# Kernel optimization log

Measured on AMD Instinct MI355X. Metric: run time of the kernel, lower is better.

The kernel has to match this reference:

```python
import jax, jax.numpy as jnp
import numpy as np

NUM_CLASSES = 80
INF = 1e8
STRIDES = (8, 16, 32, 64, 128)
REG = ((0.0, 64.0), (64.0, 128.0), (128.0, 256.0), (256.0, 512.0), (512.0, INF))
GRAY_F = (0.9, 1.1)
FM = ((128, 128), (64, 64), (32, 32), (16, 16), (8, 8))  # 1024x1024 input


def _build_level_constants():
    pts, rr, gr, st = [], [], [], []
    for (h, w), s, (lo, up) in zip(FM, STRIDES, REG):
        xs = np.arange(w, dtype=np.float32) * s
        ys = np.arange(h, dtype=np.float32) * s
        ym, xm = np.meshgrid(ys, xs, indexing='ij')
        n = h * w
        pts.append(np.stack([xm.ravel(), ym.ravel()], axis=-1))
        rr.append(np.tile(np.array([lo, up], np.float32), (n, 1)))
        gr.append(np.tile(np.array([lo * GRAY_F[0], up * GRAY_F[1]], np.float32), (n, 1)))
        st.append(np.full((n,), s, np.float32))
    cat = lambda a: jnp.asarray(np.concatenate(a, axis=0))
    return cat(pts), cat(rr), cat(gr), cat(st)


def setup_inputs() -> dict:
    key = jax.random.key(0)
    k1, k2, k3, k4 = jax.random.split(key, 4)
    B, G = 8, 100
    x0 = jax.random.uniform(k1, (B, G, 1), minval=0.0, maxval=900.0)
    y0 = jax.random.uniform(k2, (B, G, 1), minval=0.0, maxval=900.0)
    wh = jax.random.uniform(k3, (B, G, 2), minval=8.0, maxval=512.0)
    gt_bboxes = jnp.concatenate([x0, y0, wh], axis=-1)  # xywh
    gt_labels = jax.random.randint(k4, (B, G), 0, NUM_CLASSES)
    points, reg_ranges, gray_ranges, strides = _build_level_constants()
    return dict(gt_bboxes=gt_bboxes, gt_labels=gt_labels, points=points,
                reg_ranges=reg_ranges, gray_ranges=gray_ranges, strides=strides)


def _single_image(gt_bboxes, gt_labels, points, reg_ranges, gray_ranges, strides):
    # gt_bboxes [G,4] (x,y,w,h); points [P,2]; returns [P, C+4]
    px = points[:, 0:1]                      # [P,1]
    py = points[:, 1:2]
    x0 = gt_bboxes[None, :, 0]               # [1,G]
    y0 = gt_bboxes[None, :, 1]
    w = gt_bboxes[None, :, 2]
    h = gt_bboxes[None, :, 3]
    cx = x0 + w / 2.0
    cy = y0 + h / 2.0
    half = strides[:, None] / 2.0            # [P,1]

    xs = jnp.abs(px - cx) / half
    xs = jnp.where(xs >= 1.0, xs, 1.0)       # == xs*(xs>=1) + (xs<1)
    ys = jnp.abs(py - cy) / half
    ys = jnp.where(ys >= 1.0, ys, 1.0)
    scores = jnp.sqrt(1.0 / xs) * jnp.sqrt(1.0 / ys)   # [P,G]

    dx1 = px - x0
    dy1 = py - y0
    dx2 = x0 + w - 1.0 - px
    dy2 = y0 + h - 1.0 - py
    delta = jnp.stack([dx1, dy1, dx2, dy2], axis=-1)   # [P,G,4]
    delta = delta / reg_ranges[:, 1][:, None, None]

    larger = jnp.maximum(w, h)               # [1,G]
    lo, up = reg_ranges[:, 0:1], reg_ranges[:, 1:2]      # [P,1]
    glo, gup = gray_ranges[:, 0:1], gray_ranges[:, 1:2]
    hit = jnp.min(delta, axis=-1) >= 0       # [P,G]
    green = (lo <= larger) & (larger <= up) & hit
    gray = (((glo <= larger) & (larger < lo)) | ((up < larger) & (larger <= gup))) & hit

    order = jnp.argsort(scores, axis=1)      # ascending, like torch.sort
    s_scores = jnp.take_along_axis(scores, order, axis=1)
    s_labels = jnp.take_along_axis(jnp.broadcast_to(gt_labels[None, :], scores.shape), order, axis=1)
    s_green = jnp.take_along_axis(green, order, axis=1)
    s_gray = jnp.take_along_axis(gray, order, axis=1)
    s_delta = jnp.take_along_axis(delta, order[..., None], axis=1)

    P = points.shape[0]
    rows = jnp.broadcast_to(jnp.arange(P)[:, None], s_labels.shape)
    cls = jnp.zeros((P, NUM_CLASSES), scores.dtype)
    cls = cls.at[rows, s_labels].max(jnp.where(s_green, s_scores, 0.0))
    gray_hit = jnp.zeros((P, NUM_CLASSES), scores.dtype)
    gray_hit = gray_hit.at[rows, s_labels].max(s_gray.astype(scores.dtype))
    cls = jnp.where(gray_hit > 0, -1.0, cls)  # gray writes happen after green

    filt = s_scores * (s_green & ~s_gray)
    sel = jnp.argmax(filt, axis=1)            # first max, like torch.max
    reg = jnp.take_along_axis(s_delta, sel[:, None, None], axis=1)[:, 0, :]  # [P,4]
    return jnp.concatenate([cls, reg], axis=-1)


def reference(gt_bboxes, gt_labels, points, reg_ranges, gray_ranges, strides):
    f = jax.vmap(lambda b, l: _single_image(b, l, points, reg_ranges, gray_ranges, strides))
    return f(gt_bboxes, gt_labels)
```

## Files before the change

kernel.cpp:

```cpp
#include <hip/hip_runtime.h>

#define ROWF 84

__global__ __launch_bounds__(64) void lfd_assign_kernel(
    const float* __restrict__ gt_bboxes,
    const int*   __restrict__ gt_labels,
    const float* __restrict__ points,
    const float* __restrict__ reg_ranges,
    const float* __restrict__ gray_ranges,
    const float* __restrict__ strides,
    float* __restrict__ out,
    int G, int P)
{
    extern __shared__ float lds[];
    float4*   boxA  = (float4*)lds;
    float2*   ctr   = (float2*)(boxA + G);
    unsigned* clist = (unsigned*)(ctr + ((G + 1) & ~1));

    const int tid = threadIdx.x;
    const int b   = blockIdx.y;
    const int p   = blockIdx.x * 64 + tid;

    const float px  = points[p * 2 + 0];
    const float py  = points[p * 2 + 1];
    const float lo  = reg_ranges[p * 2 + 0];
    const float up  = reg_ranges[p * 2 + 1];
    const float glo = gray_ranges[p * 2 + 0];
    const float gup = gray_ranges[p * 2 + 1];
    const float inv_half = 2.0f / strides[p];
    const float inv_up   = 1.0f / up;

    bool i0 = false, gray0 = false, i1 = false, gray1 = false;
    int  lab0 = 0, lab1 = 0;
    {
        int g = tid;
        if (g < G) {
            const float4 bb = *(const float4*)(gt_bboxes + (size_t)(b * G + g) * 4);
            boxA[g] = make_float4(bb.x, bb.y, bb.x + bb.z - 1.0f, bb.y + bb.w - 1.0f);
            ctr[g]  = make_float2(bb.x + 0.5f * bb.z, bb.y + 0.5f * bb.w);
            const float larger = fmaxf(bb.z, bb.w);
            lab0 = gt_labels[b * G + g];
            const bool green = (lo <= larger) && (larger <= up);
            gray0 = ((glo <= larger) && (larger < lo)) || ((up < larger) && (larger <= gup));
            i0 = green || gray0;
        }
        g = tid + 64;
        if (g < G) {
            const float4 bb = *(const float4*)(gt_bboxes + (size_t)(b * G + g) * 4);
            boxA[g] = make_float4(bb.x, bb.y, bb.x + bb.z - 1.0f, bb.y + bb.w - 1.0f);
            ctr[g]  = make_float2(bb.x + 0.5f * bb.z, bb.y + 0.5f * bb.w);
            const float larger = fmaxf(bb.z, bb.w);
            lab1 = gt_labels[b * G + g];
            const bool green = (lo <= larger) && (larger <= up);
            gray1 = ((glo <= larger) && (larger < lo)) || ((up < larger) && (larger <= gup));
            i1 = green || gray1;
        }
    }
    const unsigned long long m0 = __ballot(i0);
    const unsigned long long m1 = __ballot(i1);
    const int c0 = __popcll(m0);
    const unsigned long long below = (1ull << tid) - 1ull;
    if (i0) clist[__popcll(m0 & below)] =
        (unsigned)tid | ((unsigned)lab0 << 8) | (gray0 ? 0x80000000u : 0u);
    if (i1) clist[c0 + __popcll(m1 & below)] =
        (unsigned)(tid + 64) | ((unsigned)lab1 << 8) | (gray1 ? 0x80000000u : 0u);
    const int ncomp = c0 + __popcll(m1);

    float4* dst4 = (float4*)(out + (size_t)(b * P + blockIdx.x * 64) * ROWF);
    const float4 z4 = make_float4(0.f, 0.f, 0.f, 0.f);
#pragma unroll
    for (int k = 0; k < 21; ++k)
        dst4[k * 64 + tid] = z4;

    const float4* ctr2 = (const float4*)ctr;
    float min_score = 1e30f; int min_g = 0;
    int g = 0;
#pragma unroll 4
    for (; g + 1 < G; g += 2) {
        const float4 c = ctr2[g >> 1];
        const float s0 = rsqrtf(fmaxf(fabsf(px - c.x) * inv_half, 1.0f) *
                                fmaxf(fabsf(py - c.y) * inv_half, 1.0f));
        const float s1 = rsqrtf(fmaxf(fabsf(px - c.z) * inv_half, 1.0f) *
                                fmaxf(fabsf(py - c.w) * inv_half, 1.0f));
        if (s0 < min_score) { min_score = s0; min_g = g; }
        if (s1 < min_score) { min_score = s1; min_g = g + 1; }
    }
    if (g < G) {
        const float2 c = ctr[g];
        const float s0 = rsqrtf(fmaxf(fabsf(px - c.x) * inv_half, 1.0f) *
                                fmaxf(fabsf(py - c.y) * inv_half, 1.0f));
        if (s0 < min_score) { min_score = s0; min_g = g; }
    }

    asm volatile("s_waitcnt vmcnt(0)" ::: "memory");

    float* myout = out + (size_t)(b * P + p) * ROWF;
    float best_score = 0.0f; int best_g = 0;
    unsigned gm0 = 0u, gm1 = 0u, gm2 = 0u;
    for (int i = 0; i < ncomp; ++i) {
        const unsigned e = clist[i];
        const int gg = (int)(e & 0xFFu);
        const float4 A = boxA[gg];
        const float d1 = px - A.x, d2 = py - A.y, d3 = A.z - px, d4 = A.w - py;
        if (fminf(fminf(d1, d2), fminf(d3, d4)) >= 0.0f) {
            const int label = (int)((e >> 8) & 0x7Fu);
            if (e & 0x80000000u) {
                if (label < 32)      gm0 |= 1u << label;
                else if (label < 64) gm1 |= 1u << (label - 32);
                else                 gm2 |= 1u << (label - 64);
            } else {
                const float2 c = ctr[gg];
                const float s = rsqrtf(fmaxf(fabsf(px - c.x) * inv_half, 1.0f) *
                                       fmaxf(fabsf(py - c.y) * inv_half, 1.0f));
                atomicMax((int*)(myout + label), __float_as_int(s));
                if (s > best_score) { best_score = s; best_g = gg; }
            }
        }
    }

    asm volatile("s_waitcnt vmcnt(0)" ::: "memory");

    while (gm0) { const int c = __ffs(gm0) - 1; myout[c]      = -1.0f; gm0 &= gm0 - 1u; }
    while (gm1) { const int c = __ffs(gm1) - 1; myout[32 + c] = -1.0f; gm1 &= gm1 - 1u; }
    while (gm2) { const int c = __ffs(gm2) - 1; myout[64 + c] = -1.0f; gm2 &= gm2 - 1u; }

    const int sel = (best_score > 0.0f) ? best_g : min_g;
    const float4 A = boxA[sel];
    *(float4*)(myout + 80) = make_float4((px - A.x) * inv_up, (py - A.y) * inv_up,
                                         (A.z - px) * inv_up, (A.w - py) * inv_up);
}

extern "C" void kernel_launch(void* const* d_in, const int* in_sizes, int n_in,
                              void* d_out, int out_size, void* d_ws, size_t ws_size,
                              hipStream_t stream) {
    const float* gt_bboxes   = (const float*)d_in[0];
    const int*   gt_labels   = (const int*)d_in[1];
    const float* points      = (const float*)d_in[2];
    const float* reg_ranges  = (const float*)d_in[3];
    const float* gray_ranges = (const float*)d_in[4];
    const float* strides     = (const float*)d_in[5];
    float* out = (float*)d_out;

    const int P = in_sizes[5];
    const int B = out_size / (P * ROWF);
    const int G = in_sizes[1] / B;

    dim3 grid(P / 64, B);
    dim3 block(64);
    const size_t shmem = (size_t)G * sizeof(float4)
                       + (size_t)((G + 1) & ~1) * sizeof(float2)
                       + (size_t)G * sizeof(unsigned);
    lfd_assign_kernel<<<grid, block, shmem, stream>>>(
        gt_bboxes, gt_labels, points, reg_ranges, gray_ranges, strides, out, G, P);
}
```

Before: 33.90 us.

## Accumulate per-class max scores in registers instead of global atomics

```diff
diff --git a/kernel.cpp b/kernel.cpp
--- a/kernel.cpp
+++ b/kernel.cpp
@@ -1,8 +1,10 @@
 #include <hip/hip_runtime.h>
 
 #define ROWF 84
+#define KSLOT 8
+#define SENT 0xFFFFFFFFu
 
-__global__ __launch_bounds__(64) void lfd_assign_kernel(
+__global__ __launch_bounds__(256, 2) void lfd_assign_kernel(
     const float* __restrict__ gt_bboxes,
     const int*   __restrict__ gt_labels,
     const float* __restrict__ points,
@@ -16,61 +18,63 @@
     float4*   boxA  = (float4*)lds;
     float2*   ctr   = (float2*)(boxA + G);
     unsigned* clist = (unsigned*)(ctr + ((G + 1) & ~1));
+    unsigned* flags = clist + G;
+    int*      s_ncomp = (int*)(flags + 128);
 
     const int tid = threadIdx.x;
     const int b   = blockIdx.y;
-    const int p   = blockIdx.x * 64 + tid;
+    const int p   = blockIdx.x * 256 + tid;
+    const bool active = (p < P);
+    const int  pc = active ? p : (P - 1);
 
-    const float px  = points[p * 2 + 0];
-    const float py  = points[p * 2 + 1];
-    const float lo  = reg_ranges[p * 2 + 0];
-    const float up  = reg_ranges[p * 2 + 1];
-    const float glo = gray_ranges[p * 2 + 0];
-    const float gup = gray_ranges[p * 2 + 1];
-    const float inv_half = 2.0f / strides[p];
+    float* myout = out + ((size_t)b * P + p) * ROWF;
+    if (active) {
+        const float4 z = make_float4(0.f, 0.f, 0.f, 0.f);
+        float4* r4 = (float4*)myout;
+#pragma unroll
+        for (int k = 0; k < 20; ++k) r4[k] = z;
+    }
+
+    const float px  = points[pc * 2 + 0];
+    const float py  = points[pc * 2 + 1];
+    const float lo  = reg_ranges[pc * 2 + 0];
+    const float up  = reg_ranges[pc * 2 + 1];
+    const float glo = gray_ranges[pc * 2 + 0];
+    const float gup = gray_ranges[pc * 2 + 1];
+    const float inv_half = 2.0f / strides[pc];
     const float inv_up   = 1.0f / up;
 
-    bool i0 = false, gray0 = false, i1 = false, gray1 = false;
-    int  lab0 = 0, lab1 = 0;
-    {
-        int g = tid;
-        if (g < G) {
-            const float4 bb = *(const float4*)(gt_bboxes + (size_t)(b * G + g) * 4);
-            boxA[g] = make_float4(bb.x, bb.y, bb.x + bb.z - 1.0f, bb.y + bb.w - 1.0f);
-            ctr[g]  = make_float2(bb.x + 0.5f * bb.z, bb.y + 0.5f * bb.w);
+    if (tid < 128) {
+        unsigned f = SENT;
+        if (tid < G) {
+            const float4 bb = *(const float4*)(gt_bboxes + ((size_t)b * G + tid) * 4);
+            boxA[tid] = make_float4(bb.x, bb.y, bb.x + bb.z - 1.0f, bb.y + bb.w - 1.0f);
+            ctr[tid]  = make_float2(bb.x + 0.5f * bb.z, bb.y + 0.5f * bb.w);
             const float larger = fmaxf(bb.z, bb.w);
-            lab0 = gt_labels[b * G + g];
+            const int lab = gt_labels[b * G + tid];
             const bool green = (lo <= larger) && (larger <= up);
-            gray0 = ((glo <= larger) && (larger < lo)) || ((up < larger) && (larger <= gup));
-            i0 = green || gray0;
+            const bool gray  = ((glo <= larger) && (larger < lo)) ||
+                               ((up < larger) && (larger <= gup));
+            if (green || gray)
+                f = (unsigned)tid | ((unsigned)lab << 8) | (gray ? 0x80000000u : 0u);
         }
-        g = tid + 64;
-        if (g < G) {
-            const float4 bb = *(const float4*)(gt_bboxes + (size_t)(b * G + g) * 4);
-            boxA[g] = make_float4(bb.x, bb.y, bb.x + bb.z - 1.0f, bb.y + bb.w - 1.0f);
-            ctr[g]  = make_float2(bb.x + 0.5f * bb.z, bb.y + 0.5f * bb.w);
-            const float larger = fmaxf(bb.z, bb.w);
-            lab1 = gt_labels[b * G + g];
-            const bool green = (lo <= larger) && (larger <= up);
-            gray1 = ((glo <= larger) && (larger < lo)) || ((up < larger) && (larger <= gup));
-            i1 = green || gray1;
-        }
+        flags[tid] = f;
     }
-    const unsigned long long m0 = __ballot(i0);
-    const unsigned long long m1 = __ballot(i1);
-    const int c0 = __popcll(m0);
-    const unsigned long long below = (1ull << tid) - 1ull;
-    if (i0) clist[__popcll(m0 & below)] =
-        (unsigned)tid | ((unsigned)lab0 << 8) | (gray0 ? 0x80000000u : 0u);
-    if (i1) clist[c0 + __popcll(m1 & below)] =
-        (unsigned)(tid + 64) | ((unsigned)lab1 << 8) | (gray1 ? 0x80000000u : 0u);
-    const int ncomp = c0 + __popcll(m1);
+    __syncthreads();
 
-    float4* dst4 = (float4*)(out + (size_t)(b * P + blockIdx.x * 64) * ROWF);
-    const float4 z4 = make_float4(0.f, 0.f, 0.f, 0.f);
-#pragma unroll
-    for (int k = 0; k < 21; ++k)
-        dst4[k * 64 + tid] = z4;
+    if (tid < 64) {
+        const unsigned f0 = flags[tid], f1 = flags[tid + 64];
+        const bool i0 = (f0 != SENT), i1 = (f1 != SENT);
+        const unsigned long long m0 = __ballot(i0);
+        const unsigned long long m1 = __ballot(i1);
+        const unsigned long long below = (1ull << tid) - 1ull;
+        const int c0 = __popcll(m0);
+        if (i0) clist[__popcll(m0 & below)] = f0;
+        if (i1) clist[c0 + __popcll(m1 & below)] = f1;
+        if (tid == 0) *s_ncomp = c0 + __popcll(m1);
+    }
+    __syncthreads();
+    const int ncomp = *s_ncomp;
 
     const float4* ctr2 = (const float4*)ctr;
     float min_score = 1e30f; int min_g = 0;
@@ -94,15 +98,20 @@
 
     asm volatile("s_waitcnt vmcnt(0)" ::: "memory");
 
-    float* myout = out + (size_t)(b * P + p) * ROWF;
-    float best_score = 0.0f; int best_g = 0;
+    int   slab[KSLOT];
+    float sval[KSLOT];
+#pragma unroll
+    for (int j = 0; j < KSLOT; ++j) { slab[j] = -1; sval[j] = 0.f; }
+    int cnt = 0; bool spill = false;
     unsigned gm0 = 0u, gm1 = 0u, gm2 = 0u;
+    float best_score = 0.f; int best_g = 0;
+
     for (int i = 0; i < ncomp; ++i) {
         const unsigned e = clist[i];
         const int gg = (int)(e & 0xFFu);
         const float4 A = boxA[gg];
         const float d1 = px - A.x, d2 = py - A.y, d3 = A.z - px, d4 = A.w - py;
-        if (fminf(fminf(d1, d2), fminf(d3, d4)) >= 0.0f) {
+        if (active && fminf(fminf(d1, d2), fminf(d3, d4)) >= 0.0f) {
             const int label = (int)((e >> 8) & 0x7Fu);
             if (e & 0x80000000u) {
                 if (label < 32)      gm0 |= 1u << label;
@@ -112,22 +121,48 @@
                 const float2 c = ctr[gg];
                 const float s = rsqrtf(fmaxf(fabsf(px - c.x) * inv_half, 1.0f) *
                                        fmaxf(fabsf(py - c.y) * inv_half, 1.0f));
-                atomicMax((int*)(myout + label), __float_as_int(s));
+                bool placed = false;
+#pragma unroll
+                for (int j = 0; j < KSLOT; ++j)
+                    if (slab[j] == label) { sval[j] = fmaxf(sval[j], s); placed = true; }
+                if (!placed) {
+                    if (cnt < KSLOT) {
+#pragma unroll
+                        for (int j = 0; j < KSLOT; ++j)
+                            if (cnt == j) { slab[j] = label; sval[j] = s; }
+                        ++cnt;
+                    } else {
+                        spill = true;
+                        atomicMax((int*)(myout + label), __float_as_int(s));
+                    }
+                }
                 if (s > best_score) { best_score = s; best_g = gg; }
             }
         }
     }
+    if (__any(spill))
+        asm volatile("s_waitcnt vmcnt(0)" ::: "memory");
 
-    asm volatile("s_waitcnt vmcnt(0)" ::: "memory");
+    if (active) {
+#pragma unroll
+        for (int j = 0; j < KSLOT; ++j) {
+            if (j < cnt) {
+                const int L = slab[j];
+                const unsigned gmask = (L < 32) ? gm0 : ((L < 64) ? gm1 : gm2);
+                if (!((gmask >> (L & 31)) & 1u))
+                    myout[L] = sval[j];
+            }
+        }
+        unsigned t;
+        t = gm0; while (t) { const int c = __ffs(t) - 1; myout[c]      = -1.0f; t &= t - 1u; }
+        t = gm1; while (t) { const int c = __ffs(t) - 1; myout[32 + c] = -1.0f; t &= t - 1u; }
+        t = gm2; while (t) { const int c = __ffs(t) - 1; myout[64 + c] = -1.0f; t &= t - 1u; }
 
-    while (gm0) { const int c = __ffs(gm0) - 1; myout[c]      = -1.0f; gm0 &= gm0 - 1u; }
-    while (gm1) { const int c = __ffs(gm1) - 1; myout[32 + c] = -1.0f; gm1 &= gm1 - 1u; }
-    while (gm2) { const int c = __ffs(gm2) - 1; myout[64 + c] = -1.0f; gm2 &= gm2 - 1u; }
-
-    const int sel = (best_score > 0.0f) ? best_g : min_g;
-    const float4 A = boxA[sel];
-    *(float4*)(myout + 80) = make_float4((px - A.x) * inv_up, (py - A.y) * inv_up,
-                                         (A.z - px) * inv_up, (A.w - py) * inv_up);
+        const int sel = (best_score > 0.f) ? best_g : min_g;
+        const float4 A = boxA[sel];
+        *(float4*)(myout + 80) = make_float4((px - A.x) * inv_up, (py - A.y) * inv_up,
+                                             (A.z - px) * inv_up, (A.w - py) * inv_up);
+    }
 }
 
 extern "C" void kernel_launch(void* const* d_in, const int* in_sizes, int n_in,
@@ -145,11 +180,13 @@
     const int B = out_size / (P * ROWF);
     const int G = in_sizes[1] / B;
 
-    dim3 grid(P / 64, B);
-    dim3 block(64);
+    dim3 grid((P + 255) / 256, B);
+    dim3 block(256);
     const size_t shmem = (size_t)G * sizeof(float4)
                        + (size_t)((G + 1) & ~1) * sizeof(float2)
-                       + (size_t)G * sizeof(unsigned);
+                       + (size_t)G * sizeof(unsigned)
+                       + 128 * sizeof(unsigned)
+                       + sizeof(int);
     lfd_assign_kernel<<<grid, block, shmem, stream>>>(
         gt_bboxes, gt_labels, points, reg_ranges, gray_ranges, strides, out, G, P);
 }
```

After: 54.45 us. 60.6% more time.
